# Performance work log

Hardware: AMD Instinct MI355X
Metric: run time of the kernel (lower is better)

Reference implementation:

```python
import jax, jax.numpy as jnp
import numpy as np

CHUNK = 128  # chunk size for the causal linear-attention recurrence
EPS = 1e-10


def _causal_numerator(q, k, v, chunk=CHUNK):
    """N_i = sum_{j<=i} (q_i . k_j) v_j, computed chunk-recurrently.

    q,k: [B,H,N,D]; v: [B,H,N,E] -> [B,H,N,E]
    """
    B, H, N, D = q.shape
    E = v.shape[-1]
    nc = N // chunk
    qc = jnp.moveaxis(q.reshape(B, H, nc, chunk, D), 2, 0)  # [nc,B,H,c,D]
    kc = jnp.moveaxis(k.reshape(B, H, nc, chunk, D), 2, 0)
    vc = jnp.moveaxis(v.reshape(B, H, nc, chunk, E), 2, 0)
    mask = jnp.tril(jnp.ones((chunk, chunk), dtype=q.dtype))  # causal within chunk

    def step(S, inp):  # S: running sum of k_j (outer) v_j -> [B,H,D,E]
        qi, ki, vi = inp
        scores = jnp.einsum('bhid,bhjd->bhij', qi, ki) * mask
        intra = jnp.einsum('bhij,bhje->bhie', scores, vi)
        inter = jnp.einsum('bhid,bhde->bhie', qi, S)
        S = S + jnp.einsum('bhjd,bhje->bhde', ki, vi)
        return S, intra + inter

    S0 = jnp.zeros((B, H, D, E), q.dtype)
    _, outs = jax.lax.scan(step, S0, (qc, kc, vc))  # [nc,B,H,c,E]
    return jnp.moveaxis(outs, 0, 2).reshape(B, H, N, E)


def _causal_denominator(q, k):
    # D_i = q_i . cumsum_j<=i k_j  -> [B,H,N]
    return jnp.einsum('bhnd,bhnd->bhn', q, jnp.cumsum(k, axis=-2))


def setup_inputs() -> dict:
    key = jax.random.key(0)
    ks = jax.random.split(key, 5)
    shape = (2, 8, 4096, 64)
    names = ['q', 'k', 'q_rot', 'k_rot', 'v']
    # feature-mapped inputs (Performer softmax features) are positive
    return {n: jax.random.uniform(ks[i], shape, dtype=jnp.float32) for i, n in enumerate(names)}


def reference(q, k, q_rot, k_rot, v):
    N = _causal_numerator(q, k, v) + _causal_numerator(q_rot, k_rot, v)
    D = _causal_denominator(q, k) + _causal_denominator(q_rot, k_rot)
    return N * (1.0 / (D + EPS))[..., None]
```

## Files before the change

kernel.cpp:

```cpp
#include <hip/hip_runtime.h>

#define SEQ 4096
#define DIM 64
#define CHUNK 128
#define NC 32
#define EPSV 1e-10f
#define KS_OFF 4194304

typedef __attribute__((ext_vector_type(8))) short s16x8;
typedef __attribute__((ext_vector_type(4))) float f32x4;

__device__ __forceinline__ unsigned short f2bf(float f) {
  unsigned int u = __float_as_uint(f);
  u += 0x7FFF + ((u >> 16) & 1);
  return (unsigned short)(u >> 16);
}
__device__ __forceinline__ float bf2f(unsigned short s) {
  return __uint_as_float(((unsigned int)s) << 16);
}

__device__ __forceinline__ void stage_nat(const float* __restrict__ gp,
                                          unsigned short* __restrict__ nat, int t) {
#pragma unroll
  for (int p = 0; p < 8; ++p) {
    int idx = t + p * 256;
    int i = idx >> 4, d4 = idx & 15;
    float4 x = ((const float4*)gp)[idx];
    ushort4 u = make_ushort4(f2bf(x.x), f2bf(x.y), f2bf(x.z), f2bf(x.w));
    *(ushort4*)&nat[i * 72 + d4 * 4] = u;
  }
}

__device__ __forceinline__ void transpose_to_T(const unsigned short* __restrict__ nat,
                                               unsigned short* __restrict__ dst, int t) {
  int L = t & 63, w = t >> 6;
#pragma unroll
  for (int it = 0; it < 4; ++it) {
    int d = L, j8 = it * 4 + w;
    s16x8 seg;
#pragma unroll
    for (int u = 0; u < 8; ++u) seg[u] = (short)nat[(j8 * 8 + u) * 72 + d];
    *(s16x8*)&dst[d * 136 + j8 * 8] = seg;
  }
}

__global__ __launch_bounds__(256) void pass_a(const float* __restrict__ k0,
                                              const float* __restrict__ k1,
                                              const float* __restrict__ v,
                                              float* __restrict__ ws) {
  __shared__ __align__(16) unsigned short skT[64 * 136];
  __shared__ __align__(16) unsigned short svT[64 * 136];
  __shared__ __align__(16) unsigned short snat[128 * 72];
  int bid = blockIdx.x;
  int m = bid >> 9, rem = bid & 511, hh = rem >> 5, c = rem & 31;
  const float* kp = (m ? k1 : k0) + (size_t)hh * SEQ * DIM + (size_t)c * CHUNK * DIM;
  const float* vp = v + (size_t)hh * SEQ * DIM + (size_t)c * CHUNK * DIM;
  int t = threadIdx.x;

  stage_nat(kp, snat, t);
  __syncthreads();
  transpose_to_T(snat, skT, t);
  __syncthreads();
  stage_nat(vp, snat, t);
  __syncthreads();
  transpose_to_T(snat, svT, t);
  __syncthreads();

  if (t < 64) {
    float s = 0.f;
    for (int it = 0; it < 16; ++it) {
      s16x8 blk = *(const s16x8*)&skT[t * 136 + it * 8];
#pragma unroll
      for (int u = 0; u < 8; ++u) s += bf2f((unsigned short)blk[u]);
    }
    ws[KS_OFF + (size_t)bid * 64 + t] = s;
  }

  int w = t >> 6, L = t & 63, g = L >> 4, cL = L & 15;
  f32x4 acc[4];
#pragma unroll
  for (int ct = 0; ct < 4; ++ct) acc[ct] = (f32x4){0.f, 0.f, 0.f, 0.f};
#pragma unroll
  for (int ks = 0; ks < 4; ++ks) {
    s16x8 aF = *(const s16x8*)&svT[(w * 16 + cL) * 136 + ks * 32 + g * 8];
#pragma unroll
    for (int ct = 0; ct < 4; ++ct) {
      s16x8 bF = *(const s16x8*)&skT[(ct * 16 + cL) * 136 + ks * 32 + g * 8];
      acc[ct] = __builtin_amdgcn_mfma_f32_16x16x32_bf16(aF, bF, acc[ct], 0, 0, 0);
    }
  }
  float* Sp = ws + (size_t)bid * 4096;
#pragma unroll
  for (int ct = 0; ct < 4; ++ct)
#pragma unroll
    for (int r = 0; r < 4; ++r)
      Sp[(size_t)(w * 16 + g * 4 + r) * 64 + ct * 16 + cL] = acc[ct][r];
}

__global__ __launch_bounds__(256) void pass_b(float* __restrict__ ws) {
  int t = blockIdx.x * 256 + threadIdx.x;
  if (blockIdx.x < 512) {
    int mh = t >> 12, de = t & 4095;
    float* p = ws + (size_t)mh * NC * 4096 + de;
    float run = 0.f;
    for (int c = 0; c < NC; ++c) {
      float x = p[(size_t)c * 4096];
      p[(size_t)c * 4096] = run;
      run += x;
    }
  } else {
    int t2 = t - 512 * 256;
    int mh = t2 >> 6, d = t2 & 63;
    float* p = ws + KS_OFF + (size_t)mh * NC * 64 + d;
    float run = 0.f;
    for (int c = 0; c < NC; ++c) {
      float x = p[(size_t)c * 64];
      p[(size_t)c * 64] = run;
      run += x;
    }
  }
}

__global__ __launch_bounds__(256) void pass_c(const float* __restrict__ q0,
                                              const float* __restrict__ q1,
                                              const float* __restrict__ k0,
                                              const float* __restrict__ k1,
                                              const float* __restrict__ v,
                                              const float* __restrict__ ws,
                                              float* __restrict__ out) {
  __shared__ __align__(16) unsigned short sq[128 * 72];
  __shared__ __align__(16) unsigned short skl[128 * 72];
  __shared__ __align__(16) unsigned short svT[64 * 136];
  __shared__ __align__(16) unsigned short sU[5120];
  __shared__ float sden[128];
  __shared__ float skpref[64];

  int hh = blockIdx.x >> 5, c = blockIdx.x & 31;
  int t = threadIdx.x;
  int w = t >> 6, L = t & 63, g = L >> 4, cL = L & 15;
  size_t off = (size_t)hh * SEQ * DIM + (size_t)c * CHUNK * DIM;
  int rt_of[2] = {w, 7 - w};

  stage_nat(v + off, skl, t);
  __syncthreads();
  transpose_to_T(skl, svT, t);

  f32x4 accO[2][4];
#pragma unroll
  for (int a = 0; a < 2; ++a)
#pragma unroll
    for (int b = 0; b < 4; ++b) accO[a][b] = (f32x4){0.f, 0.f, 0.f, 0.f};
  float denfrag[2][4] = {};
  float denqk = 0.f;

  for (int m = 0; m < 2; ++m) {
    const float* qp = (m ? q1 : q0) + off;
    const float* kp = (m ? k1 : k0) + off;
    const float* Sp = ws + (size_t)(m * 512 + hh * 32 + c) * 4096;
    const float* Kp = ws + KS_OFF + (size_t)(m * 512 + hh * 32 + c) * 64;

    __syncthreads();
    stage_nat(qp, sq, t);
    stage_nat(kp, skl, t);
#pragma unroll
    for (int pass = 0; pass < 4; ++pass) {
      int idx = t + pass * 256;
      int e = idx >> 4, d4 = idx & 15;
      float4 ss = ((const float4*)Sp)[idx];
      ushort4 us = make_ushort4(f2bf(ss.x), f2bf(ss.y), f2bf(ss.z), f2bf(ss.w));
      *(ushort4*)&sU[e * 72 + d4 * 4] = us;
    }
    if (t < 64) skpref[t] = Kp[t];
    __syncthreads();

    s16x8 aq[2][2];
#pragma unroll
    for (int ti = 0; ti < 2; ++ti) {
      int row = rt_of[ti] * 16 + cL;
      aq[ti][0] = *(const s16x8*)&sq[row * 72 + g * 8];
      aq[ti][1] = *(const s16x8*)&sq[row * 72 + 32 + g * 8];
    }

    if (t < 128) {
      float s = 0.f;
      for (int it = 0; it < 8; ++it) {
        s16x8 blk = *(const s16x8*)&sq[t * 72 + it * 8];
#pragma unroll
        for (int u = 0; u < 8; ++u) s += bf2f((unsigned short)blk[u]) * skpref[it * 8 + u];
      }
      denqk += s;
    }

#pragma unroll
    for (int h = 0; h < 2; ++h) {
#pragma unroll
      for (int et = 0; et < 4; ++et) {
        s16x8 bS = *(const s16x8*)&sU[(et * 16 + cL) * 72 + h * 32 + g * 8];
        accO[0][et] = __builtin_amdgcn_mfma_f32_16x16x32_bf16(aq[0][h], bS, accO[0][et], 0, 0, 0);
        accO[1][et] = __builtin_amdgcn_mfma_f32_16x16x32_bf16(aq[1][h], bS, accO[1][et], 0, 0, 0);
      }
    }
    __syncthreads();

    for (int s = 0; s <= (7 - w) >> 1; ++s) {
      s16x8 bK[2][2];
#pragma unroll
      for (int ct01 = 0; ct01 < 2; ++ct01) {
        int jrow = (2 * s + ct01) * 16 + cL;
        bK[ct01][0] = *(const s16x8*)&skl[jrow * 72 + g * 8];
        bK[ct01][1] = *(const s16x8*)&skl[jrow * 72 + 32 + g * 8];
      }
#pragma unroll
      for (int ti = 0; ti < 2; ++ti) {
        int rt = rt_of[ti];
        if (2 * s > rt) continue;
        int rowbase = rt * 16 + g * 4;
#pragma unroll
        for (int ct01 = 0; ct01 < 2; ++ct01) {
          int jt = 2 * s + ct01;
          if (jt > rt) {
#pragma unroll
            for (int r = 0; r < 4; ++r) sU[(rowbase + r) * 40 + ct01 * 16 + cL] = 0;
          } else {
            f32x4 C = (f32x4){0.f, 0.f, 0.f, 0.f};
            C = __builtin_amdgcn_mfma_f32_16x16x32_bf16(aq[ti][0], bK[ct01][0], C, 0, 0, 0);
            C = __builtin_amdgcn_mfma_f32_16x16x32_bf16(aq[ti][1], bK[ct01][1], C, 0, 0, 0);
            if (jt == rt) {
#pragma unroll
              for (int r = 0; r < 4; ++r)
                if (cL > g * 4 + r) C[r] = 0.f;
            }
#pragma unroll
            for (int r = 0; r < 4; ++r) {
              denfrag[ti][r] += C[r];
              sU[(rowbase + r) * 40 + ct01 * 16 + cL] = f2bf(C[r]);
            }
          }
        }
      }
      asm volatile("s_waitcnt lgkmcnt(0)" ::: "memory");

      s16x8 bV[4];
#pragma unroll
      for (int et = 0; et < 4; ++et)
        bV[et] = *(const s16x8*)&svT[(et * 16 + cL) * 136 + s * 32 + g * 8];
#pragma unroll
      for (int ti = 0; ti < 2; ++ti) {
        if (2 * s > rt_of[ti]) continue;
        s16x8 aP = *(const s16x8*)&sU[(rt_of[ti] * 16 + cL) * 40 + g * 8];
#pragma unroll
        for (int et = 0; et < 4; ++et)
          accO[ti][et] = __builtin_amdgcn_mfma_f32_16x16x32_bf16(aP, bV[et], accO[ti][et], 0, 0, 0);
      }
    }
  }

  if (t < 128) sden[t] = denqk;
  __syncthreads();

  float* op = out + off;
#pragma unroll
  for (int ti = 0; ti < 2; ++ti) {
#pragma unroll
    for (int r = 0; r < 4; ++r) {
      float vs = denfrag[ti][r];
      vs += __shfl_xor(vs, 1);
      vs += __shfl_xor(vs, 2);
      vs += __shfl_xor(vs, 4);
      vs += __shfl_xor(vs, 8);
      int row = rt_of[ti] * 16 + g * 4 + r;
      float inv = 1.f / (sden[row] + vs + EPSV);
#pragma unroll
      for (int et = 0; et < 4; ++et)
        op[(size_t)row * 64 + et * 16 + cL] = accO[ti][et][r] * inv;
    }
  }
}

extern "C" void kernel_launch(void* const* d_in, const int* in_sizes, int n_in,
                              void* d_out, int out_size, void* d_ws, size_t ws_size,
                              hipStream_t stream) {
  const float* q  = (const float*)d_in[0];
  const float* k  = (const float*)d_in[1];
  const float* qr = (const float*)d_in[2];
  const float* kr = (const float*)d_in[3];
  const float* v  = (const float*)d_in[4];
  float* out = (float*)d_out;
  float* ws  = (float*)d_ws;

  hipLaunchKernelGGL(pass_a, dim3(1024), dim3(256), 0, stream, k, kr, v, ws);
  hipLaunchKernelGGL(pass_b, dim3(520), dim3(256), 0, stream, ws);
  hipLaunchKernelGGL(pass_c, dim3(512), dim3(256), 0, stream, q, qr, k, kr, v, ws, out);
}
```

Baseline: 143.7 us.

## Store chunk states as bf16 and load q/k fragments directly from global

Pass A now writes the per-chunk KV state in bf16 instead of fp32, which halves workspace traffic. Pass B scans packed bf16 pairs with all loads issued up front. Pass C builds q and k MFMA fragments straight from global memory rather than staging them in LDS, and computes the q·cumsum(k) denominator from those registers. This cuts LDS footprint and staging syncs but rounds the prefix sums to bf16 and issues redundant uncoalesced global loads of k inside the loop.

```diff
diff --git a/kernel.cpp b/kernel.cpp
--- a/kernel.cpp
+++ b/kernel.cpp
@@ -5,7 +5,7 @@
 #define CHUNK 128
 #define NC 32
 #define EPSV 1e-10f
-#define KS_OFF 4194304
+#define KS_OFF 2097152
 
 typedef __attribute__((ext_vector_type(8))) short s16x8;
 typedef __attribute__((ext_vector_type(4))) float f32x4;
@@ -17,6 +17,12 @@
 }
 __device__ __forceinline__ float bf2f(unsigned short s) {
   return __uint_as_float(((unsigned int)s) << 16);
+}
+__device__ __forceinline__ s16x8 pack8(float4 a, float4 b) {
+  s16x8 r;
+  r[0] = (short)f2bf(a.x); r[1] = (short)f2bf(a.y); r[2] = (short)f2bf(a.z); r[3] = (short)f2bf(a.w);
+  r[4] = (short)f2bf(b.x); r[5] = (short)f2bf(b.y); r[6] = (short)f2bf(b.z); r[7] = (short)f2bf(b.w);
+  return r;
 }
 
 __device__ __forceinline__ void stage_nat(const float* __restrict__ gp,
@@ -89,34 +95,43 @@
       acc[ct] = __builtin_amdgcn_mfma_f32_16x16x32_bf16(aF, bF, acc[ct], 0, 0, 0);
     }
   }
-  float* Sp = ws + (size_t)bid * 4096;
+  unsigned short* Sp = (unsigned short*)ws + (size_t)bid * 4096;
 #pragma unroll
   for (int ct = 0; ct < 4; ++ct)
 #pragma unroll
     for (int r = 0; r < 4; ++r)
-      Sp[(size_t)(w * 16 + g * 4 + r) * 64 + ct * 16 + cL] = acc[ct][r];
+      Sp[(size_t)(w * 16 + g * 4 + r) * 64 + ct * 16 + cL] = f2bf(acc[ct][r]);
 }
 
 __global__ __launch_bounds__(256) void pass_b(float* __restrict__ ws) {
-  int t = blockIdx.x * 256 + threadIdx.x;
-  if (blockIdx.x < 512) {
-    int mh = t >> 12, de = t & 4095;
-    float* p = ws + (size_t)mh * NC * 4096 + de;
+  int t = threadIdx.x;
+  if (blockIdx.x < 256) {
+    int gid = blockIdx.x * 256 + t;
+    int mh = gid >> 11, de2 = gid & 2047;
+    unsigned int* p = (unsigned int*)ws + (size_t)mh * NC * 2048 + de2;
+    unsigned int x[NC];
+#pragma unroll
+    for (int c = 0; c < NC; ++c) x[c] = p[(size_t)c * 2048];
+    float r0 = 0.f, r1 = 0.f;
+#pragma unroll
+    for (int c = 0; c < NC; ++c) {
+      unsigned int xc = x[c];
+      p[(size_t)c * 2048] = (unsigned int)f2bf(r0) | ((unsigned int)f2bf(r1) << 16);
+      r0 += bf2f((unsigned short)(xc & 0xFFFF));
+      r1 += bf2f((unsigned short)(xc >> 16));
+    }
+  } else {
+    int gid = (blockIdx.x - 256) * 256 + t;
+    int mh = gid >> 6, d = gid & 63;
+    float* p = ws + KS_OFF + (size_t)mh * NC * 64 + d;
+    float x[NC];
+#pragma unroll
+    for (int c = 0; c < NC; ++c) x[c] = p[(size_t)c * 64];
     float run = 0.f;
+#pragma unroll
     for (int c = 0; c < NC; ++c) {
-      float x = p[(size_t)c * 4096];
-      p[(size_t)c * 4096] = run;
-      run += x;
-    }
-  } else {
-    int t2 = t - 512 * 256;
-    int mh = t2 >> 6, d = t2 & 63;
-    float* p = ws + KS_OFF + (size_t)mh * NC * 64 + d;
-    float run = 0.f;
-    for (int c = 0; c < NC; ++c) {
-      float x = p[(size_t)c * 64];
       p[(size_t)c * 64] = run;
-      run += x;
+      run += x[c];
     }
   }
 }
@@ -128,12 +143,10 @@
                                               const float* __restrict__ v,
                                               const float* __restrict__ ws,
                                               float* __restrict__ out) {
-  __shared__ __align__(16) unsigned short sq[128 * 72];
-  __shared__ __align__(16) unsigned short skl[128 * 72];
   __shared__ __align__(16) unsigned short svT[64 * 136];
-  __shared__ __align__(16) unsigned short sU[5120];
+  __shared__ __align__(16) unsigned short sun[128 * 72];
+  __shared__ float skpref[64];
   __shared__ float sden[128];
-  __shared__ float skpref[64];
 
   int hh = blockIdx.x >> 5, c = blockIdx.x & 31;
   int t = threadIdx.x;
@@ -141,9 +154,9 @@
   size_t off = (size_t)hh * SEQ * DIM + (size_t)c * CHUNK * DIM;
   int rt_of[2] = {w, 7 - w};
 
-  stage_nat(v + off, skl, t);
-  __syncthreads();
-  transpose_to_T(skl, svT, t);
+  stage_nat(v + off, sun, t);
+  __syncthreads();
+  transpose_to_T(sun, svT, t);
 
   f32x4 accO[2][4];
 #pragma unroll
@@ -151,51 +164,55 @@
 #pragma unroll
     for (int b = 0; b < 4; ++b) accO[a][b] = (f32x4){0.f, 0.f, 0.f, 0.f};
   float denfrag[2][4] = {};
-  float denqk = 0.f;
+  float denp[2] = {0.f, 0.f};
+
+  const unsigned short* Sbase = (const unsigned short*)ws;
 
   for (int m = 0; m < 2; ++m) {
     const float* qp = (m ? q1 : q0) + off;
     const float* kp = (m ? k1 : k0) + off;
-    const float* Sp = ws + (size_t)(m * 512 + hh * 32 + c) * 4096;
+    const unsigned short* Sp = Sbase + (size_t)(m * 512 + hh * 32 + c) * 4096;
     const float* Kp = ws + KS_OFF + (size_t)(m * 512 + hh * 32 + c) * 64;
 
     __syncthreads();
-    stage_nat(qp, sq, t);
-    stage_nat(kp, skl, t);
-#pragma unroll
-    for (int pass = 0; pass < 4; ++pass) {
-      int idx = t + pass * 256;
-      int e = idx >> 4, d4 = idx & 15;
-      float4 ss = ((const float4*)Sp)[idx];
-      ushort4 us = make_ushort4(f2bf(ss.x), f2bf(ss.y), f2bf(ss.z), f2bf(ss.w));
-      *(ushort4*)&sU[e * 72 + d4 * 4] = us;
+#pragma unroll
+    for (int p2 = 0; p2 < 2; ++p2) {
+      int idx = t + p2 * 256;
+      int e = idx >> 3, seg = idx & 7;
+      *(s16x8*)&sun[e * 72 + seg * 8] = *(const s16x8*)&Sp[idx * 8];
     }
     if (t < 64) skpref[t] = Kp[t];
     __syncthreads();
 
+    float kpf[2][8];
+#pragma unroll
+    for (int h = 0; h < 2; ++h) {
+      float4 c0 = *(const float4*)&skpref[h * 32 + g * 8];
+      float4 c1 = *(const float4*)&skpref[h * 32 + g * 8 + 4];
+      kpf[h][0] = c0.x; kpf[h][1] = c0.y; kpf[h][2] = c0.z; kpf[h][3] = c0.w;
+      kpf[h][4] = c1.x; kpf[h][5] = c1.y; kpf[h][6] = c1.z; kpf[h][7] = c1.w;
+    }
+
     s16x8 aq[2][2];
 #pragma unroll
     for (int ti = 0; ti < 2; ++ti) {
       int row = rt_of[ti] * 16 + cL;
-      aq[ti][0] = *(const s16x8*)&sq[row * 72 + g * 8];
-      aq[ti][1] = *(const s16x8*)&sq[row * 72 + 32 + g * 8];
-    }
-
-    if (t < 128) {
-      float s = 0.f;
-      for (int it = 0; it < 8; ++it) {
-        s16x8 blk = *(const s16x8*)&sq[t * 72 + it * 8];
-#pragma unroll
-        for (int u = 0; u < 8; ++u) s += bf2f((unsigned short)blk[u]) * skpref[it * 8 + u];
-      }
-      denqk += s;
+#pragma unroll
+      for (int h = 0; h < 2; ++h) {
+        const float* qa = qp + row * 64 + h * 32 + g * 8;
+        float4 a0 = *(const float4*)qa;
+        float4 a1 = *(const float4*)(qa + 4);
+        denp[ti] += a0.x * kpf[h][0] + a0.y * kpf[h][1] + a0.z * kpf[h][2] + a0.w * kpf[h][3]
+                  + a1.x * kpf[h][4] + a1.y * kpf[h][5] + a1.z * kpf[h][6] + a1.w * kpf[h][7];
+        aq[ti][h] = pack8(a0, a1);
+      }
     }
 
 #pragma unroll
     for (int h = 0; h < 2; ++h) {
 #pragma unroll
       for (int et = 0; et < 4; ++et) {
-        s16x8 bS = *(const s16x8*)&sU[(et * 16 + cL) * 72 + h * 32 + g * 8];
+        s16x8 bS = *(const s16x8*)&sun[(et * 16 + cL) * 72 + h * 32 + g * 8];
         accO[0][et] = __builtin_amdgcn_mfma_f32_16x16x32_bf16(aq[0][h], bS, accO[0][et], 0, 0, 0);
         accO[1][et] = __builtin_amdgcn_mfma_f32_16x16x32_bf16(aq[1][h], bS, accO[1][et], 0, 0, 0);
       }
@@ -207,8 +224,13 @@
 #pragma unroll
       for (int ct01 = 0; ct01 < 2; ++ct01) {
         int jrow = (2 * s + ct01) * 16 + cL;
-        bK[ct01][0] = *(const s16x8*)&skl[jrow * 72 + g * 8];
-        bK[ct01][1] = *(const s16x8*)&skl[jrow * 72 + 32 + g * 8];
+#pragma unroll
+        for (int h = 0; h < 2; ++h) {
+          const float* ka = kp + jrow * 64 + h * 32 + g * 8;
+          float4 b0 = *(const float4*)ka;
+          float4 b1 = *(const float4*)(ka + 4);
+          bK[ct01][h] = pack8(b0, b1);
+        }
       }
 #pragma unroll
       for (int ti = 0; ti < 2; ++ti) {
@@ -220,7 +242,7 @@
           int jt = 2 * s + ct01;
           if (jt > rt) {
 #pragma unroll
-            for (int r = 0; r < 4; ++r) sU[(rowbase + r) * 40 + ct01 * 16 + cL] = 0;
+            for (int r = 0; r < 4; ++r) sun[(rowbase + r) * 40 + ct01 * 16 + cL] = 0;
           } else {
             f32x4 C = (f32x4){0.f, 0.f, 0.f, 0.f};
             C = __builtin_amdgcn_mfma_f32_16x16x32_bf16(aq[ti][0], bK[ct01][0], C, 0, 0, 0);
@@ -233,7 +255,7 @@
 #pragma unroll
             for (int r = 0; r < 4; ++r) {
               denfrag[ti][r] += C[r];
-              sU[(rowbase + r) * 40 + ct01 * 16 + cL] = f2bf(C[r]);
+              sun[(rowbase + r) * 40 + ct01 * 16 + cL] = f2bf(C[r]);
             }
           }
         }
@@ -247,7 +269,7 @@
 #pragma unroll
       for (int ti = 0; ti < 2; ++ti) {
         if (2 * s > rt_of[ti]) continue;
-        s16x8 aP = *(const s16x8*)&sU[(rt_of[ti] * 16 + cL) * 40 + g * 8];
+        s16x8 aP = *(const s16x8*)&sun[(rt_of[ti] * 16 + cL) * 40 + g * 8];
 #pragma unroll
         for (int et = 0; et < 4; ++et)
           accO[ti][et] = __builtin_amdgcn_mfma_f32_16x16x32_bf16(aP, bV[et], accO[ti][et], 0, 0, 0);
@@ -255,7 +277,15 @@
     }
   }
 
-  if (t < 128) sden[t] = denqk;
+#pragma unroll
+  for (int ti = 0; ti < 2; ++ti) {
+    denp[ti] += __shfl_xor(denp[ti], 16);
+    denp[ti] += __shfl_xor(denp[ti], 32);
+  }
+  if (L < 16) {
+    sden[rt_of[0] * 16 + L] = denp[0];
+    sden[rt_of[1] * 16 + L] = denp[1];
+  }
   __syncthreads();
 
   float* op = out + off;
@@ -289,6 +319,6 @@
   float* ws  = (float*)d_ws;
 
   hipLaunchKernelGGL(pass_a, dim3(1024), dim3(256), 0, stream, k, kr, v, ws);
-  hipLaunchKernelGGL(pass_b, dim3(520), dim3(256), 0, stream, ws);
+  hipLaunchKernelGGL(pass_b, dim3(264), dim3(256), 0, stream, ws);
   hipLaunchKernelGGL(pass_c, dim3(512), dim3(256), 0, stream, q, qr, k, kr, v, ws, out);
 }
```

New measurement: 140.4 us. 1.02x faster.
